# Kernel optimization log

Hardware: AMD Instinct MI355X
Metric: run time of the kernel (lower is better)

The kernel has to match this reference:

```python
import jax, jax.numpy as jnp
import numpy as np

N = 100000
E = 1600000
NFEAT, NHID, NCLASS = 128, 128, 40


def setup_inputs() -> dict:
    key = jax.random.key(0)
    ks = jax.random.split(key, 12)
    inp = {
        "x": jax.random.normal(ks[0], (N, NFEAT), dtype=jnp.float32),
        "src": jax.random.randint(ks[1], (E,), 0, N, dtype=jnp.int32),
        "tgt": jax.random.randint(ks[2], (E,), 0, N, dtype=jnp.int32),
        "Mtgt": jax.random.uniform(ks[3], (E,), dtype=jnp.float32),  # per-edge aggregation weights (sparse Mtgt values)
    }
    s = 1.0 / np.sqrt(NHID)
    inp["W0"] = jax.random.uniform(ks[4], (NFEAT, NHID), minval=-s, maxval=s, dtype=jnp.float32)
    inp["b0"] = jnp.zeros((NHID,), jnp.float32)
    inp["W1"] = jax.random.uniform(ks[5], (NHID, NHID), minval=-s, maxval=s, dtype=jnp.float32)
    inp["b1"] = jnp.zeros((NHID,), jnp.float32)
    inp["W2"] = jax.random.uniform(ks[6], (NHID, NHID), minval=-s, maxval=s, dtype=jnp.float32)
    inp["b2"] = jnp.zeros((NHID,), jnp.float32)
    inp["W3"] = jax.random.uniform(ks[7], (NHID, NCLASS), minval=-s, maxval=s, dtype=jnp.float32)
    inp["b3"] = jnp.zeros((NCLASS,), jnp.float32)
    return inp


def _gcn_layer(x, W, b, src, tgt, w_edge):
    # GraphConvolution: dense transform then edge gather -> weighted scatter-add to tgt
    h = x @ W                                  # [N, out]
    msg = h[src] * w_edge[:, None]             # [E, out]
    agg = jax.ops.segment_sum(msg, tgt, num_segments=N)  # [N, out]
    return agg + b


def reference(x, src, tgt, Mtgt, W0, b0, W1, b1, W2, b2, W3, b3):
    # eval mode: dropout is identity
    h = jax.nn.relu(_gcn_layer(x, W0, b0, src, tgt, Mtgt))
    for (W, b) in ((W1, b1), (W2, b2)):
        r = h
        h = jax.nn.relu(_gcn_layer(h, W, b, src, tgt, Mtgt)) + r
    h = _gcn_layer(h, W3, b3, src, tgt, Mtgt)
    return jax.nn.log_softmax(h, axis=1)
```

## Files before the change

### kernel.cpp

```cpp
#include <hip/hip_runtime.h>
#include <hip/hip_fp16.h>
#include <math.h>

#define NF 128
#define NC 40

typedef unsigned short bfraw;
typedef float f32x4 __attribute__((ext_vector_type(4)));
typedef short s16x8 __attribute__((ext_vector_type(8)));

__device__ __forceinline__ float bfLo(unsigned u) {
  return __uint_as_float(u << 16);
}
__device__ __forceinline__ float bfHi(unsigned u) {
  return __uint_as_float(u & 0xffff0000u);
}
__device__ __forceinline__ unsigned short f2bf(float f) {
  unsigned u = __float_as_uint(f);
  u += 0x7fff + ((u >> 16) & 1);
  return (unsigned short)(u >> 16);
}
__device__ __forceinline__ unsigned short f2h15(float f) {
  __half h = __float2half(f);
  __half_raw hr = static_cast<__half_raw>(h);
  return (unsigned short)(hr.x & 0x7FFF);
}
__device__ __forceinline__ float h15tof(unsigned rec) {
  __half_raw hr;
  hr.x = (unsigned short)(rec & 0x7FFF);
  __half h = static_cast<__half>(hr);
  return __half2float(h);
}


__global__ __launch_bounds__(256) void count_kernel(const int* __restrict__ tgt,
                                                    int* __restrict__ cnt, int e) {
  int i = blockIdx.x * 256 + threadIdx.x;
  if (i < e) atomicAdd(&cnt[__builtin_nontemporal_load(&tgt[i])], 1);
}

__global__ __launch_bounds__(1024) void scan1_kernel(const int* __restrict__ cnt,
                                                     int* __restrict__ rp,
                                                     int* __restrict__ bsum, int n) {
  __shared__ int wsum[16];
  int tid = threadIdx.x, lane = tid & 63, wid = tid >> 6;
  int i = blockIdx.x * 1024 + tid;
  int v = (i < n) ? cnt[i] : 0;
  int x = v;
  #pragma unroll
  for (int off = 1; off < 64; off <<= 1) {
    int t = __shfl_up(x, off);
    if (lane >= off) x += t;
  }
  if (lane == 63) wsum[wid] = x;
  __syncthreads();
  if (wid == 0) {
    int ws = (lane < 16) ? wsum[lane] : 0;
    int y = ws;
    #pragma unroll
    for (int off = 1; off < 16; off <<= 1) {
      int t = __shfl_up(y, off);
      if (lane >= off) y += t;
    }
    if (lane < 16) wsum[lane] = y - ws;
  }
  __syncthreads();
  int incl = x + wsum[wid];
  if (i < n) rp[i] = incl - v;
  if (tid == 1023) bsum[blockIdx.x] = incl;
}

__global__ __launch_bounds__(1024) void scan2_kernel(int* __restrict__ bsum, int nb,
                                                     int* __restrict__ rp_n) {
  __shared__ int wsum[16];
  int tid = threadIdx.x, lane = tid & 63, wid = tid >> 6;
  int v = (tid < nb) ? bsum[tid] : 0;
  int x = v;
  #pragma unroll
  for (int off = 1; off < 64; off <<= 1) {
    int t = __shfl_up(x, off);
    if (lane >= off) x += t;
  }
  if (lane == 63) wsum[wid] = x;
  __syncthreads();
  if (wid == 0) {
    int ws = (lane < 16) ? wsum[lane] : 0;
    int y = ws;
    #pragma unroll
    for (int off = 1; off < 16; off <<= 1) {
      int t = __shfl_up(y, off);
      if (lane >= off) y += t;
    }
    if (lane < 16) wsum[lane] = y - ws;
  }
  __syncthreads();
  int incl = x + wsum[wid];
  if (tid < nb) bsum[tid] = incl - v;
  if (tid == 1023) *rp_n = incl;
}

__global__ __launch_bounds__(256) void scan3_kernel(int* __restrict__ rp,
                                                    int* __restrict__ cursor,
                                                    const int* __restrict__ bsum, int n) {
  int i = blockIdx.x * 256 + threadIdx.x;
  if (i < n) {
    int v = rp[i] + bsum[i >> 10];
    rp[i] = v;
    cursor[i] = v;
  }
}

__global__ __launch_bounds__(256) void fill_kernel(const int* __restrict__ src,
                                                   const int* __restrict__ tgt,
                                                   const float* __restrict__ mw,
                                                   int* __restrict__ cursor,
                                                   unsigned* __restrict__ ecsr,
                                                   int e, int n) {
  int part = blockIdx.x & 7;
  int nset = gridDim.x >> 3;
  int lo = (int)(((long long)n * part) >> 3);
  int hi = (int)(((long long)n * (part + 1)) >> 3);
  int stride = nset * 256;
  for (int i = (blockIdx.x >> 3) * 256 + threadIdx.x; i < e; i += stride) {
    int t = __builtin_nontemporal_load(&tgt[i]);
    if (t >= lo && t < hi) {
      int pos = atomicAdd(&cursor[t], 1);
      unsigned s = (unsigned)__builtin_nontemporal_load(&src[i]);
      float w = __builtin_nontemporal_load(&mw[i]);
      ecsr[pos] = (s << 15) | f2h15(w);
    }
  }
}


__global__ __launch_bounds__(256) void wpack_kernel(const float* __restrict__ W0,
                                                    const float* __restrict__ W1,
                                                    const float* __restrict__ W2,
                                                    bfraw* __restrict__ Wb) {
  int id = blockIdx.x * 256 + threadIdx.x;
  if (id >= 3 * NF * NF) return;
  int w = id >> 14;
  int el = id & 16383;
  int k = el >> 7;
  int col = el & 127;
  const float* W = (w == 0) ? W0 : ((w == 1) ? W1 : W2);
  float v = W[k * NF + col];
  int ct = col >> 4;
  int kt = k >> 5;
  int g = (k & 31) >> 3;
  int j = k & 7;
  int ln = g * 16 + (col & 15);
  Wb[((((w * 8 + ct) * 4 + kt) * 64) + ln) * 8 + j] = f2bf(v);
}

__global__ __launch_bounds__(256) void wpack40_kernel(const float* __restrict__ W3,
                                                      bfraw* __restrict__ Wb3) {
  int id = blockIdx.x * 256 + threadIdx.x;
  if (id >= NF * 48) return;
  int k = id / 48;
  int col = id % 48;
  float v = (col < NC) ? W3[k * NC + col] : 0.f;
  int ct = col >> 4;
  int kt = k >> 5;
  int g = (k & 31) >> 3;
  int j = k & 7;
  int ln = g * 16 + (col & 15);
  Wb3[(((ct * 4 + kt) * 64) + ln) * 8 + j] = f2bf(v);
}


template <bool INF32>
__global__ __launch_bounds__(256) void gemm128_mfma_kernel(const void* __restrict__ Xv,
                                                           const bfraw* __restrict__ Wb,
                                                           bfraw* __restrict__ Tb, int n) {
  __shared__ __align__(16) bfraw stage[4][16][NF + 8];
  int wv = threadIdx.x >> 6;
  int lane = threadIdx.x & 63;
  int rowBase = blockIdx.x * 64 + wv * 16;
  int arow = rowBase + (lane & 15);
  int g = lane >> 4;
  bool rv = arow < n;

  s16x8 afrag[4];
  #pragma unroll
  for (int kt = 0; kt < 4; ++kt) {
    s16x8 t = {0, 0, 0, 0, 0, 0, 0, 0};
    if (rv) {
      if (INF32) {
        const float* xr = (const float*)Xv + (size_t)arow * NF + kt * 32 + g * 8;
        float4 x0 = *(const float4*)xr;
        float4 x1 = *(const float4*)(xr + 4);
        t[0] = (short)f2bf(x0.x); t[1] = (short)f2bf(x0.y);
        t[2] = (short)f2bf(x0.z); t[3] = (short)f2bf(x0.w);
        t[4] = (short)f2bf(x1.x); t[5] = (short)f2bf(x1.y);
        t[6] = (short)f2bf(x1.z); t[7] = (short)f2bf(x1.w);
      } else {
        t = *(const s16x8*)((const bfraw*)Xv + (size_t)arow * NF + kt * 32 + g * 8);
      }
    }
    afrag[kt] = t;
  }

  #pragma unroll
  for (int ct = 0; ct < 8; ++ct) {
    f32x4 acc = {0.f, 0.f, 0.f, 0.f};
    #pragma unroll
    for (int kt = 0; kt < 4; ++kt) {
      s16x8 b = *(const s16x8*)&Wb[(((ct * 4 + kt) * 64) + lane) * 8];
      acc = __builtin_amdgcn_mfma_f32_16x16x32_bf16(afrag[kt], b, acc, 0, 0, 0);
    }
    #pragma unroll
    for (int r = 0; r < 4; ++r) {
      stage[wv][g * 4 + r][ct * 16 + (lane & 15)] = f2bf(acc[r]);
    }
  }
  __syncthreads();
  int rr = lane >> 2;
  int cc = (lane & 3) * 32;
  int grow = rowBase + rr;
  if (grow < n) {
    #pragma unroll
    for (int q = 0; q < 4; ++q) {
      uint4 v = *(const uint4*)&stage[wv][rr][cc + q * 8];
      *(uint4*)&Tb[(size_t)grow * NF + cc + q * 8] = v;
    }
  }
}


__global__ __launch_bounds__(256) void gemm40_mfma_kernel(const bfraw* __restrict__ X,
                                                          const bfraw* __restrict__ Wb3,
                                                          bfraw* __restrict__ T40, int n) {
  __shared__ __align__(16) bfraw stage[4][16][72];
  int wv = threadIdx.x >> 6;
  int lane = threadIdx.x & 63;
  int rowBase = blockIdx.x * 64 + wv * 16;
  int arow = rowBase + (lane & 15);
  int g = lane >> 4;
  bool rv = arow < n;

  s16x8 afrag[4];
  #pragma unroll
  for (int kt = 0; kt < 4; ++kt) {
    s16x8 t = {0, 0, 0, 0, 0, 0, 0, 0};
    if (rv) t = *(const s16x8*)&X[(size_t)arow * NF + kt * 32 + g * 8];
    afrag[kt] = t;
  }

  #pragma unroll
  for (int ct = 0; ct < 3; ++ct) {
    f32x4 acc = {0.f, 0.f, 0.f, 0.f};
    #pragma unroll
    for (int kt = 0; kt < 4; ++kt) {
      s16x8 b = *(const s16x8*)&Wb3[(((ct * 4 + kt) * 64) + lane) * 8];
      acc = __builtin_amdgcn_mfma_f32_16x16x32_bf16(afrag[kt], b, acc, 0, 0, 0);
    }
    #pragma unroll
    for (int r = 0; r < 4; ++r) {
      stage[wv][g * 4 + r][ct * 16 + (lane & 15)] = f2bf(acc[r]);
    }
  }
  #pragma unroll
  for (int r = 0; r < 4; ++r) stage[wv][g * 4 + r][48 + (lane & 15)] = 0;
  __syncthreads();
  int rr = lane >> 2;
  int cc = (lane & 3) * 16;
  int grow = rowBase + rr;
  if (grow < n) {
    uint4 v0 = *(const uint4*)&stage[wv][rr][cc];
    uint4 v1 = *(const uint4*)&stage[wv][rr][cc + 8];
    *(uint4*)&T40[(size_t)grow * 64 + cc] = v0;
    *(uint4*)&T40[(size_t)grow * 64 + cc + 8] = v1;
  }
}


template <bool RELU, bool RES, bool BIAS, bool OUTBF>
__global__ __launch_bounds__(256) void agg128_kernel(const bfraw* __restrict__ Tb,
                                                     const int* __restrict__ rp,
                                                     const unsigned* __restrict__ ecsr,
                                                     const float* __restrict__ bias,
                                                     const bfraw* __restrict__ Hres,
                                                     void* __restrict__ HoutV, int n) {
  int node = (blockIdx.x * 256 + threadIdx.x) >> 6;
  int lane = threadIdx.x & 63;
  if (node >= n) return;
  int st = lane >> 4;
  int fl = lane & 15;
  int beg = rp[node], end = rp[node + 1];
  float a[8];
  #pragma unroll
  for (int i = 0; i < 8; ++i) a[i] = 0.f;
  int eidx = beg + st;
  for (; eidx + 4 < end; eidx += 8) {
    unsigned e0 = __builtin_nontemporal_load(&ecsr[eidx]);
    unsigned e1 = __builtin_nontemporal_load(&ecsr[eidx + 4]);
    float w0 = h15tof(e0);
    float w1 = h15tof(e1);
    uint4 q0 = *(const uint4*)&Tb[(size_t)(e0 >> 15) * NF + fl * 8];
    uint4 q1 = *(const uint4*)&Tb[(size_t)(e1 >> 15) * NF + fl * 8];
    a[0] = fmaf(w0, bfLo(q0.x), a[0]); a[1] = fmaf(w0, bfHi(q0.x), a[1]);
    a[2] = fmaf(w0, bfLo(q0.y), a[2]); a[3] = fmaf(w0, bfHi(q0.y), a[3]);
    a[4] = fmaf(w0, bfLo(q0.z), a[4]); a[5] = fmaf(w0, bfHi(q0.z), a[5]);
    a[6] = fmaf(w0, bfLo(q0.w), a[6]); a[7] = fmaf(w0, bfHi(q0.w), a[7]);
    a[0] = fmaf(w1, bfLo(q1.x), a[0]); a[1] = fmaf(w1, bfHi(q1.x), a[1]);
    a[2] = fmaf(w1, bfLo(q1.y), a[2]); a[3] = fmaf(w1, bfHi(q1.y), a[3]);
    a[4] = fmaf(w1, bfLo(q1.z), a[4]); a[5] = fmaf(w1, bfHi(q1.z), a[5]);
    a[6] = fmaf(w1, bfLo(q1.w), a[6]); a[7] = fmaf(w1, bfHi(q1.w), a[7]);
  }
  if (eidx < end) {
    unsigned e0 = __builtin_nontemporal_load(&ecsr[eidx]);
    float w0 = h15tof(e0);
    uint4 q0 = *(const uint4*)&Tb[(size_t)(e0 >> 15) * NF + fl * 8];
    a[0] = fmaf(w0, bfLo(q0.x), a[0]); a[1] = fmaf(w0, bfHi(q0.x), a[1]);
    a[2] = fmaf(w0, bfLo(q0.y), a[2]); a[3] = fmaf(w0, bfHi(q0.y), a[3]);
    a[4] = fmaf(w0, bfLo(q0.z), a[4]); a[5] = fmaf(w0, bfHi(q0.z), a[5]);
    a[6] = fmaf(w0, bfLo(q0.w), a[6]); a[7] = fmaf(w0, bfHi(q0.w), a[7]);
  }
  #pragma unroll
  for (int i = 0; i < 8; ++i) {
    a[i] += __shfl_xor(a[i], 16);
    a[i] += __shfl_xor(a[i], 32);
  }
  if (st == 0) {
    if (BIAS) {
      float4 b0 = *(const float4*)&bias[fl * 8];
      float4 b1 = *(const float4*)&bias[fl * 8 + 4];
      a[0] += b0.x; a[1] += b0.y; a[2] += b0.z; a[3] += b0.w;
      a[4] += b1.x; a[5] += b1.y; a[6] += b1.z; a[7] += b1.w;
    }
    if (RELU) {
      #pragma unroll
      for (int i = 0; i < 8; ++i) a[i] = fmaxf(a[i], 0.f);
    }
    if (RES) {
      uint4 r = *(const uint4*)&Hres[(size_t)node * NF + fl * 8];
      a[0] += bfLo(r.x); a[1] += bfHi(r.x);
      a[2] += bfLo(r.y); a[3] += bfHi(r.y);
      a[4] += bfLo(r.z); a[5] += bfHi(r.z);
      a[6] += bfLo(r.w); a[7] += bfHi(r.w);
    }
    if (OUTBF) {
      bfraw* Hout = (bfraw*)HoutV;
      uint4 o;
      o.x = ((unsigned)f2bf(a[1]) << 16) | f2bf(a[0]);
      o.y = ((unsigned)f2bf(a[3]) << 16) | f2bf(a[2]);
      o.z = ((unsigned)f2bf(a[5]) << 16) | f2bf(a[4]);
      o.w = ((unsigned)f2bf(a[7]) << 16) | f2bf(a[6]);
      *(uint4*)&Hout[(size_t)node * NF + fl * 8] = o;
    } else {
      float* Hout = (float*)HoutV;
      float4 o0, o1;
      o0.x = a[0]; o0.y = a[1]; o0.z = a[2]; o0.w = a[3];
      o1.x = a[4]; o1.y = a[5]; o1.z = a[6]; o1.w = a[7];
      *(float4*)&Hout[(size_t)node * NF + fl * 8] = o0;
      *(float4*)&Hout[(size_t)node * NF + fl * 8 + 4] = o1;
    }
  }
}


__global__ __launch_bounds__(256) void agg40_lsm_kernel(const bfraw* __restrict__ T40,
                                                        const int* __restrict__ rp,
                                                        const unsigned* __restrict__ ecsr,
                                                        const float* __restrict__ bias,
                                                        float* __restrict__ out, int n) {
  int node = (blockIdx.x * 256 + threadIdx.x) >> 6;
  int lane = threadIdx.x & 63;
  if (node >= n) return;
  int st = lane >> 4;
  int fl = lane & 15;
  int beg = rp[node], end = rp[node + 1];
  float a0 = 0.f, a1 = 0.f, a2 = 0.f, a3 = 0.f;
  int eidx = beg + st;
  for (; eidx + 4 < end; eidx += 8) {
    unsigned e0 = __builtin_nontemporal_load(&ecsr[eidx]);
    unsigned e1 = __builtin_nontemporal_load(&ecsr[eidx + 4]);
    float w0 = h15tof(e0);
    float w1 = h15tof(e1);
    uint2 q0 = *(const uint2*)&T40[(size_t)(e0 >> 15) * 64 + fl * 4];
    uint2 q1 = *(const uint2*)&T40[(size_t)(e1 >> 15) * 64 + fl * 4];
    a0 = fmaf(w0, bfLo(q0.x), a0); a1 = fmaf(w0, bfHi(q0.x), a1);
    a2 = fmaf(w0, bfLo(q0.y), a2); a3 = fmaf(w0, bfHi(q0.y), a3);
    a0 = fmaf(w1, bfLo(q1.x), a0); a1 = fmaf(w1, bfHi(q1.x), a1);
    a2 = fmaf(w1, bfLo(q1.y), a2); a3 = fmaf(w1, bfHi(q1.y), a3);
  }
  if (eidx < end) {
    unsigned e0 = __builtin_nontemporal_load(&ecsr[eidx]);
    float w0 = h15tof(e0);
    uint2 q0 = *(const uint2*)&T40[(size_t)(e0 >> 15) * 64 + fl * 4];
    a0 = fmaf(w0, bfLo(q0.x), a0); a1 = fmaf(w0, bfHi(q0.x), a1);
    a2 = fmaf(w0, bfLo(q0.y), a2); a3 = fmaf(w0, bfHi(q0.y), a3);
  }
  a0 += __shfl_xor(a0, 16); a0 += __shfl_xor(a0, 32);
  a1 += __shfl_xor(a1, 16); a1 += __shfl_xor(a1, 32);
  a2 += __shfl_xor(a2, 16); a2 += __shfl_xor(a2, 32);
  a3 += __shfl_xor(a3, 16); a3 += __shfl_xor(a3, 32);
  if (st == 0) {
    bool v = fl < 10;
    if (v) {
      float4 b = *(const float4*)&bias[fl * 4];
      a0 += b.x; a1 += b.y; a2 += b.z; a3 += b.w;
    }
    float lm = v ? fmaxf(fmaxf(a0, a1), fmaxf(a2, a3)) : -INFINITY;
    #pragma unroll
    for (int off = 1; off < 16; off <<= 1) lm = fmaxf(lm, __shfl_xor(lm, off));
    float ls = v ? (expf(a0 - lm) + expf(a1 - lm) + expf(a2 - lm) + expf(a3 - lm)) : 0.f;
    #pragma unroll
    for (int off = 1; off < 16; off <<= 1) ls += __shfl_xor(ls, off);
    float lse = lm + logf(ls);
    if (v) {
      float4 o;
      o.x = a0 - lse; o.y = a1 - lse; o.z = a2 - lse; o.w = a3 - lse;
      *(float4*)&out[(size_t)node * NC + fl * 4] = o;
    }
  }
}


extern "C" void kernel_launch(void* const* d_in, const int* in_sizes, int n_in,
                              void* d_out, int out_size, void* d_ws, size_t ws_size,
                              hipStream_t stream) {
  const float* x   = (const float*)d_in[0];
  const int*   src = (const int*)d_in[1];
  const int*   tgt = (const int*)d_in[2];
  const float* mw  = (const float*)d_in[3];
  const float* W0  = (const float*)d_in[4];
  const float* b0  = (const float*)d_in[5];
  const float* W1  = (const float*)d_in[6];
  const float* b1  = (const float*)d_in[7];
  const float* W2  = (const float*)d_in[8];
  const float* b2  = (const float*)d_in[9];
  const float* W3  = (const float*)d_in[10];
  const float* b3  = (const float*)d_in[11];
  int n = in_sizes[0] / NF;
  int e = in_sizes[1];
  float* out = (float*)d_out;

  char* ws = (char*)d_ws;
  size_t nbB = (((size_t)n * NF * sizeof(bfraw)) + 255) / 256 * 256;
  bfraw* bufT  = (bfraw*)(ws);
  bfraw* bufH0 = (bfraw*)(ws + nbB);
  bfraw* bufH1 = (bfraw*)(ws + 2 * nbB);
  char* p = ws + 3 * nbB;
  bfraw* Wb = (bfraw*)p;
  p += (((3 * 8 + 3) * 4 * 64 * 8 * sizeof(bfraw)) + 255) / 256 * 256;
  int* rp = (int*)p;      p += (((size_t)(n + 1) * 4) + 255) / 256 * 256;
  int* fill = (int*)p;    p += (((size_t)n * 4) + 255) / 256 * 256;
  int* bsum = (int*)p;    p += 4096;
  unsigned* ecsr = (unsigned*)p;

  bfraw* Wb3 = Wb + 3 * 8 * 4 * 64 * 8;

  hipMemsetAsync(fill, 0, (size_t)n * 4, stream);
  int eb = (e + 255) / 256;
  int nb1 = (n + 1023) / 1024;
  count_kernel<<<eb, 256, 0, stream>>>(tgt, fill, e);
  scan1_kernel<<<nb1, 1024, 0, stream>>>(fill, rp, bsum, n);
  scan2_kernel<<<1, 1024, 0, stream>>>(bsum, nb1, &rp[n]);
  scan3_kernel<<<(n + 255) / 256, 256, 0, stream>>>(rp, fill, bsum, n);
  fill_kernel<<<8 * 256, 256, 0, stream>>>(src, tgt, mw, fill, ecsr, e, n);
  wpack_kernel<<<(3 * NF * NF + 255) / 256, 256, 0, stream>>>(W0, W1, W2, Wb);
  wpack40_kernel<<<(NF * 48 + 255) / 256, 256, 0, stream>>>(W3, Wb3);

  int gb = (n + 63) / 64;
  int ab = (n + 3) / 4;
  gemm128_mfma_kernel<true><<<gb, 256, 0, stream>>>(x, Wb, bufT, n);
  agg128_kernel<true, false, true, true><<<ab, 256, 0, stream>>>(
      bufT, rp, ecsr, b0, nullptr, bufH0, n);
  gemm128_mfma_kernel<false><<<gb, 256, 0, stream>>>(bufH0, Wb + 8 * 4 * 64 * 8, bufT, n);
  agg128_kernel<true, true, true, true><<<ab, 256, 0, stream>>>(
      bufT, rp, ecsr, b1, bufH0, bufH1, n);
  gemm128_mfma_kernel<false><<<gb, 256, 0, stream>>>(bufH1, Wb + 2 * 8 * 4 * 64 * 8, bufT, n);
  agg128_kernel<true, true, true, true><<<ab, 256, 0, stream>>>(
      bufT, rp, ecsr, b2, bufH1, bufH0, n);
  gemm40_mfma_kernel<<<gb, 256, 0, stream>>>(bufH0, Wb3, bufT, n);
  agg40_lsm_kernel<<<ab, 256, 0, stream>>>(bufT, rp, ecsr, b3, out, n);
}
```

Measured before the change: 488.5 us.

## Bin edges by target partition during counting to avoid repeated edge scans

The separate count kernel and the fill kernel are replaced by a two-pass scheme. The first pass counts in-degrees and also buckets each packed edge (target, src, fp15 weight) into per-block, per-partition slabs using wave ballots and shared-memory counters. The second pass walks only the slab for its partition and scatters edges into CSR. Previously the fill kernel re-read the whole target array eight times, and this change removes that. The cost is writing and reading a scratch slab that reuses the hidden-buffer workspace, and any bucket holding more than SCAP edges is silently truncated, so skewed graphs would lose edges.

```diff
diff --git a/kernel.cpp b/kernel.cpp
--- a/kernel.cpp
+++ b/kernel.cpp
@@ -4,6 +4,8 @@
 
 #define NF 128
 #define NC 40
+#define NBLK 512
+#define SCAP 1024
 
 typedef unsigned short bfraw;
 typedef float f32x4 __attribute__((ext_vector_type(4)));
@@ -33,11 +35,77 @@
 }
 
 
-__global__ __launch_bounds__(256) void count_kernel(const int* __restrict__ tgt,
-                                                    int* __restrict__ cnt, int e) {
-  int i = blockIdx.x * 256 + threadIdx.x;
-  if (i < e) atomicAdd(&cnt[__builtin_nontemporal_load(&tgt[i])], 1);
-}
+__global__ __launch_bounds__(256) void p1_kernel(const int* __restrict__ src,
+                                                 const int* __restrict__ tgt,
+                                                 const float* __restrict__ mw,
+                                                 int* __restrict__ cnt,
+                                                 int* __restrict__ slabcnt,
+                                                 long long* __restrict__ slab,
+                                                 int e, int n) {
+  __shared__ int lcnt[8];
+  int B = blockIdx.x;
+  int tid = threadIdx.x;
+  int lane = tid & 63;
+  if (tid < 8) lcnt[tid] = 0;
+  __syncthreads();
+  int lo = (int)(((long long)e * B) / NBLK);
+  int hi = (int)(((long long)e * (B + 1)) / NBLK);
+  unsigned long long below = (lane == 0) ? 0ULL : ((~0ULL) >> (64 - lane));
+  long long* myslab = slab + (size_t)B * 8 * SCAP;
+  for (int i0 = lo; i0 < hi; i0 += 256) {
+    int i = i0 + tid;
+    bool active = i < hi;
+    int t = 0, sr = 0;
+    float w = 0.f;
+    if (active) {
+      t = __builtin_nontemporal_load(&tgt[i]);
+      sr = __builtin_nontemporal_load(&src[i]);
+      w = __builtin_nontemporal_load(&mw[i]);
+      atomicAdd(&cnt[t], 1);
+    }
+    int pp = active ? (int)(((long long)t * 8) / n) : -1;
+    long long v = ((long long)t << 32) |
+                  (long long)(((unsigned)sr << 15) | f2h15(w));
+    #pragma unroll
+    for (int q = 0; q < 8; ++q) {
+      unsigned long long m = __ballot(pp == q);
+      if (pp == q) {
+        int leader = __ffsll((unsigned long long)m) - 1;
+        int base = 0;
+        if (lane == leader) base = atomicAdd(&lcnt[q], (int)__popcll(m));
+        base = __shfl(base, leader);
+        int pos = base + (int)__popcll(m & below);
+        if (pos < SCAP) myslab[(size_t)q * SCAP + pos] = v;
+      }
+    }
+  }
+  __syncthreads();
+  if (tid < 8) {
+    int c = lcnt[tid];
+    slabcnt[B * 8 + tid] = (c < SCAP) ? c : SCAP;
+  }
+}
+
+
+__global__ __launch_bounds__(256) void p2_kernel(const long long* __restrict__ slab,
+                                                 const int* __restrict__ slabcnt,
+                                                 int* __restrict__ cursor,
+                                                 unsigned* __restrict__ ecsr) {
+  int p = blockIdx.x & 7;
+  int nsub = gridDim.x >> 3;
+  int bsub = blockIdx.x >> 3;
+  for (int B = bsub; B < NBLK; B += nsub) {
+    int cb = slabcnt[B * 8 + p];
+    const long long* sb = slab + ((size_t)B * 8 + p) * SCAP;
+    for (int i = threadIdx.x; i < cb; i += 256) {
+      long long v = __builtin_nontemporal_load(&sb[i]);
+      int t = (int)(v >> 32);
+      int pos = atomicAdd(&cursor[t], 1);
+      ecsr[pos] = (unsigned)(v & 0xffffffffLL);
+    }
+  }
+}
+
 
 __global__ __launch_bounds__(1024) void scan1_kernel(const int* __restrict__ cnt,
                                                      int* __restrict__ rp,
@@ -107,28 +175,6 @@
     int v = rp[i] + bsum[i >> 10];
     rp[i] = v;
     cursor[i] = v;
-  }
-}
-
-__global__ __launch_bounds__(256) void fill_kernel(const int* __restrict__ src,
-                                                   const int* __restrict__ tgt,
-                                                   const float* __restrict__ mw,
-                                                   int* __restrict__ cursor,
-                                                   unsigned* __restrict__ ecsr,
-                                                   int e, int n) {
-  int part = blockIdx.x & 7;
-  int nset = gridDim.x >> 3;
-  int lo = (int)(((long long)n * part) >> 3);
-  int hi = (int)(((long long)n * (part + 1)) >> 3);
-  int stride = nset * 256;
-  for (int i = (blockIdx.x >> 3) * 256 + threadIdx.x; i < e; i += stride) {
-    int t = __builtin_nontemporal_load(&tgt[i]);
-    if (t >= lo && t < hi) {
-      int pos = atomicAdd(&cursor[t], 1);
-      unsigned s = (unsigned)__builtin_nontemporal_load(&src[i]);
-      float w = __builtin_nontemporal_load(&mw[i]);
-      ecsr[pos] = (s << 15) | f2h15(w);
-    }
   }
 }
 
@@ -442,26 +488,27 @@
   bfraw* bufT  = (bfraw*)(ws);
   bfraw* bufH0 = (bfraw*)(ws + nbB);
   bfraw* bufH1 = (bfraw*)(ws + 2 * nbB);
+  long long* slab = (long long*)(ws + nbB);
   char* p = ws + 3 * nbB;
   bfraw* Wb = (bfraw*)p;
   p += (((3 * 8 + 3) * 4 * 64 * 8 * sizeof(bfraw)) + 255) / 256 * 256;
   int* rp = (int*)p;      p += (((size_t)(n + 1) * 4) + 255) / 256 * 256;
   int* fill = (int*)p;    p += (((size_t)n * 4) + 255) / 256 * 256;
   int* bsum = (int*)p;    p += 4096;
+  int* slabcnt = (int*)p; p += ((NBLK * 8 * 4) + 255) / 256 * 256;
   unsigned* ecsr = (unsigned*)p;
 
   bfraw* Wb3 = Wb + 3 * 8 * 4 * 64 * 8;
 
   hipMemsetAsync(fill, 0, (size_t)n * 4, stream);
-  int eb = (e + 255) / 256;
   int nb1 = (n + 1023) / 1024;
-  count_kernel<<<eb, 256, 0, stream>>>(tgt, fill, e);
+  wpack_kernel<<<(3 * NF * NF + 255) / 256, 256, 0, stream>>>(W0, W1, W2, Wb);
+  wpack40_kernel<<<(NF * 48 + 255) / 256, 256, 0, stream>>>(W3, Wb3);
+  p1_kernel<<<NBLK, 256, 0, stream>>>(src, tgt, mw, fill, slabcnt, slab, e, n);
   scan1_kernel<<<nb1, 1024, 0, stream>>>(fill, rp, bsum, n);
   scan2_kernel<<<1, 1024, 0, stream>>>(bsum, nb1, &rp[n]);
   scan3_kernel<<<(n + 255) / 256, 256, 0, stream>>>(rp, fill, bsum, n);
-  fill_kernel<<<8 * 256, 256, 0, stream>>>(src, tgt, mw, fill, ecsr, e, n);
-  wpack_kernel<<<(3 * NF * NF + 255) / 256, 256, 0, stream>>>(W0, W1, W2, Wb);
-  wpack40_kernel<<<(NF * 48 + 255) / 256, 256, 0, stream>>>(W3, Wb3);
+  p2_kernel<<<NBLK, 256, 0, stream>>>(slab, slabcnt, fill, ecsr);
 
   int gb = (n + 63) / 64;
   int ab = (n + 3) / 4;
```

After: 489.4 us. No clear change (+0.2%).
